# Performance work log

Measured on AMD Instinct MI355X. Metric: run time of the kernel, lower is better.

Reference implementation:

```python
import jax, jax.numpy as jnp
import numpy as np

C, FF, NH = 128, 2048, 8
B, D, H, W = 1, 16, 16, 16
EPS = 1e-5

def setup_inputs() -> dict:
    key = jax.random.key(0)
    ks = jax.random.split(key, 20)
    s = 0.02
    inp = {
        'x': jax.random.normal(ks[0], (B, C, D, H, W), jnp.float32),
        'Wq': jax.random.normal(ks[1], (C, C), jnp.float32) * s,
        'bq': jnp.zeros((C,), jnp.float32),
        'Wk': jax.random.normal(ks[2], (C, C), jnp.float32) * s,
        'bk': jnp.zeros((C,), jnp.float32),
        'Wv': jax.random.normal(ks[3], (C, C), jnp.float32) * s,
        'bv': jnp.zeros((C,), jnp.float32),
        'Wo': jax.random.normal(ks[4], (C, C), jnp.float32) * s,
        'bo': jnp.zeros((C,), jnp.float32),
        'W1': jax.random.normal(ks[5], (FF, C), jnp.float32) * s,
        'b1': jnp.zeros((FF,), jnp.float32),
        'W2': jax.random.normal(ks[6], (C, FF), jnp.float32) * s,
        'b2': jnp.zeros((C,), jnp.float32),
        'g1': jnp.ones((C,), jnp.float32),
        'be1': jnp.zeros((C,), jnp.float32),
        'g2': jnp.ones((C,), jnp.float32),
        'be2': jnp.zeros((C,), jnp.float32),
    }
    return inp

def _layernorm(t, g, b):
    # normalize over last (channel) dim, biased variance like torch LayerNorm
    m = jnp.mean(t, axis=-1, keepdims=True)
    v = jnp.mean(jnp.square(t - m), axis=-1, keepdims=True)
    return (t - m) * jax.lax.rsqrt(v + EPS) * g + b

def reference(x, Wq, bq, Wk, bk, Wv, bv, Wo, bo, W1, b1, W2, b2, g1, be1, g2, be2):
    b_, c, d, h, w = x.shape
    n = d * h * w
    hd = c // NH
    xf = x.reshape(b_, c, n)  # [B,C,N]
    # 1x1 conv3d == per-voxel linear over channels
    q = jnp.einsum('oc,bcn->bon', Wq, xf) + bq[:, None]
    k = jnp.einsum('oc,bcn->bon', Wk, xf) + bk[:, None]
    v = jnp.einsum('oc,bcn->bon', Wv, xf) + bv[:, None]
    q = q.reshape(b_, NH, hd, n)
    k = k.reshape(b_, NH, hd, n)
    v = v.reshape(b_, NH, hd, n)
    scores = jnp.einsum('bhcd,bhce->bhde', q, k) / (hd ** 0.5)  # [B,NH,N,N]
    probs = jax.nn.softmax(scores, axis=-1)
    attn = jnp.einsum('bhde,bhce->bhcd', probs, v).reshape(b_, c, n)
    attn = jnp.einsum('oc,bcn->bon', Wo, attn) + bo[:, None]
    x1 = xf + attn  # residual (dropout = identity at eval)
    x1 = _layernorm(x1.transpose(0, 2, 1), g1, be1)  # [B,N,C]
    hmid = jax.nn.relu(jnp.einsum('fc,bnc->bnf', W1, x1) + b1)
    ffn = jnp.einsum('cf,bnf->bnc', W2, hmid) + b2
    x2 = _layernorm(x1 + ffn, g2, be2)
    return x2.transpose(0, 2, 1).reshape(b_, c, d, h, w)
```

## Files before the change

kernel.cpp:

```cpp
#include <hip/hip_runtime.h>
#include <hip/hip_bf16.h>

typedef __hip_bfloat16 bf16;
typedef short short8 __attribute__((ext_vector_type(8)));
typedef float f32x4 __attribute__((ext_vector_type(4)));

#define C_   128
#define N_   4096
#define NH_  8
#define HD_  16
#define FF_  2048
#define SCALE_Q 0.360673760222241f

__device__ __forceinline__ unsigned short f2bf_bits(float f) {
    bf16 h = __float2bfloat16(f);
    return *reinterpret_cast<unsigned short*>(&h);
}
__device__ __forceinline__ unsigned int pack_trunc(float lo, float hi) {
    return (__float_as_uint(hi) & 0xffff0000u) | (__float_as_uint(lo) >> 16);
}
__device__ __forceinline__ short f2bf_trunc(float f) {
    return (short)(__float_as_uint(f) >> 16);
}
__device__ __forceinline__ float bfs2f(short s) {
    return __uint_as_float(((unsigned int)(unsigned short)s) << 16);
}
__device__ __forceinline__ float fast_exp2(float x) {
    return __builtin_amdgcn_exp2f(x);
}
__device__ __forceinline__ f32x4 mfma16(short8 a, short8 b, f32x4 c) {
    return __builtin_amdgcn_mfma_f32_16x16x32_bf16(a, b, c, 0, 0, 0);
}

__global__ void __launch_bounds__(256) k_prep(
    const float* __restrict__ Wq, const float* __restrict__ Wk,
    const float* __restrict__ Wv, const float* __restrict__ Wo,
    const float* __restrict__ W1, const float* __restrict__ W2,
    const float* __restrict__ x,
    bf16* __restrict__ Wqkvf, bf16* __restrict__ Wof,
    bf16* __restrict__ W1f, bf16* __restrict__ W2f,
    bf16* __restrict__ xTf)
{
    __shared__ float xs[4][512];
    const int tid = threadIdx.x, wave = tid >> 6, lane = tid & 63;
    const int gw = blockIdx.x * 4 + wave;
    const int q = lane >> 4;

    if (gw < 1152) {
        const float* src; bf16* dst; int K, otile, kch, blk;
        if (gw < 96)        { src = 0;  dst = Wqkvf; K = 128;  otile = gw >> 2;          kch = gw & 3;  blk = gw; }
        else if (gw < 128)  { int i = gw - 96;  src = Wo; dst = Wof;  K = 128;  otile = i >> 2; kch = i & 3;  blk = i; }
        else if (gw < 640)  { int i = gw - 128; src = W1; dst = W1f;  K = 128;  otile = i >> 2; kch = i & 3;  blk = i; }
        else                { int i = gw - 640; src = W2; dst = W2f;  K = 2048; otile = i >> 6; kch = i & 63; blk = i; }
        const int o = otile * 16 + (lane & 15);
        const int k0 = kch * 32 + 4 * q;
        const float* row;
        if (gw < 96) {
            row = (o < 128) ? (Wq + o * 128) : (o < 256) ? (Wk + (o - 128) * 128)
                                             : (Wv + (o - 256) * 128);
        } else {
            row = src + (size_t)o * K;
        }
        const float4 A = *(const float4*)(row + k0);
        const float4 B = *(const float4*)(row + k0 + 16);
        short8 v;
        v[0] = f2bf_bits(A.x); v[1] = f2bf_bits(B.x);
        v[2] = f2bf_bits(A.y); v[3] = f2bf_bits(B.y);
        v[4] = f2bf_bits(A.z); v[5] = f2bf_bits(B.z);
        v[6] = f2bf_bits(A.w); v[7] = f2bf_bits(B.w);
        *(short8*)((short*)dst + (size_t)blk * 512 + lane * 8) = v;
    } else {
        const int i = gw - 1152;
        const int n0 = (i >> 2) << 4, c0 = (i & 3) << 5;
        float* S = xs[wave];
        const int cl = lane & 31, ns = (lane >> 5) << 3;
        const float* p = x + (size_t)(c0 + cl) * N_ + n0 + ns;
        *(float4*)(S + cl * 16 + ns)     = *(const float4*)(p);
        *(float4*)(S + cl * 16 + ns + 4) = *(const float4*)(p + 4);
        short8 v;
        #pragma unroll
        for (int j = 0; j < 8; ++j) {
            const int ko = ((j & 1) << 4) + 4 * q + (j >> 1);
            v[j] = f2bf_bits(S[ko * 16 + (lane & 15)]);
        }
        *(short8*)((short*)xTf + (size_t)i * 512 + lane * 8) = v;
    }
}

__global__ void __launch_bounds__(256) k_qkv(
    const bf16* __restrict__ xTf, const bf16* __restrict__ Wqkvf,
    const float* __restrict__ bq, const float* __restrict__ bk, const float* __restrict__ bv,
    bf16* __restrict__ qf, bf16* __restrict__ kf, bf16* __restrict__ vf)
{
    __shared__ short tb[4][512];
    const int tid = threadIdx.x, wave = tid >> 6, lane = tid & 63;
    const int col = lane & 15, quad = lane >> 4;
    const int gw = blockIdx.x * 4 + wave;
    const int rt = gw / 24, ct = gw % 24;
    f32x4 acc = {};
    #pragma unroll
    for (int c = 0; c < 4; ++c) {
        short8 a = *(const short8*)(xTf + ((size_t)(rt * 4 + c) << 9) + lane * 8);
        short8 b = *(const short8*)(Wqkvf + ((size_t)(ct * 4 + c) << 9) + lane * 8);
        acc = mfma16(a, b, acc);
    }
    short* T = tb[wave];
    if (ct < 8) {
        const float bb = bq[ct * 16 + col];
        #pragma unroll
        for (int r = 0; r < 4; ++r)
            T[(col >> 3) * 128 + (quad * 4 + r) * 8 + (col & 7)] =
                f2bf_trunc((acc[r] + bb) * SCALE_Q);
    } else if (ct < 16) {
        const float bb = bk[(ct - 8) * 16 + col];
        #pragma unroll
        for (int r = 0; r < 4; ++r)
            T[(col >> 3) * 128 + (quad * 4 + r) * 8 + (col & 7)] =
                f2bf_trunc(acc[r] + bb);
    } else {
        const float bb = bv[(ct - 16) * 16 + col];
        #pragma unroll
        for (int r = 0; r < 4; ++r) {
            const int ko = quad * 4 + r;
            T[(ko >> 3) * 128 + col * 8 + (ko & 7)] = f2bf_trunc(acc[r] + bb);
        }
    }
    if (lane < 32) {
        short8 w = *(const short8*)(T + lane * 8);
        short* dst;
        if (ct < 8)       dst = (short*)qf + ((ct << 8) + rt) * 256;
        else if (ct < 16) dst = (short*)kf + (((ct - 8) << 8) + rt) * 256;
        else              dst = (short*)vf + ((((ct - 16) << 7) + (rt >> 1)) << 9) + (rt & 1) * 256;
        *(short8*)(dst + lane * 8) = w;
    }
}

__global__ void __launch_bounds__(256)
attn_kernel(const bf16* __restrict__ qf, const bf16* __restrict__ kf,
            const bf16* __restrict__ vf, bf16* __restrict__ af)
{
    __shared__ __align__(16) union {
        unsigned int P[4][2][320];
        float comb[4][64][8];
    } sh;
    const int tid = threadIdx.x, wave = tid >> 6, lane = tid & 63;
    const int col = lane & 15, quad = lane >> 4;
    const int gw = blockIdx.x;
    const int h  = gw >> 8;
    const int tile = gw & 255;
    const f32x4 zero = {};

    short8 aq = {};
    if (quad < 2)
        aq = *(const short8*)(qf + ((size_t)((h << 8) + tile) << 8) + lane * 8);

    f32x4 accO0 = {}, accO1 = {};
    float L[4] = {0.f, 0.f, 0.f, 0.f};

    const int kbeg = wave << 10;
    short* P0 = (short*)&sh.P[wave][0][0];
    short* P1 = (short*)&sh.P[wave][1][0];

    for (int i = 0; i < 32; i += 2) {
        const int mA = kbeg + (i << 5);
        const int mB = mA + 32;

        short8 bkA0 = {}, bkA1 = {}, bkB0 = {}, bkB1 = {};
        if (quad < 2) {
            const bf16* ka = kf + ((size_t)((h << 8) + (mA >> 4)) << 8) + lane * 8;
            bkA0 = *(const short8*)(ka);
            bkA1 = *(const short8*)(ka + 256);
            bkB0 = *(const short8*)(ka + 512);
            bkB1 = *(const short8*)(ka + 768);
        }
        f32x4 s0 = mfma16(aq, bkA0, zero);
        f32x4 s1 = mfma16(aq, bkA1, zero);
        f32x4 s2 = mfma16(aq, bkB0, zero);
        f32x4 s3 = mfma16(aq, bkB1, zero);
        #pragma unroll
        for (int r = 0; r < 4; ++r) {
            const float p0 = fast_exp2(s0[r]);
            const float p1 = fast_exp2(s1[r]);
            const float p2 = fast_exp2(s2[r]);
            const float p3 = fast_exp2(s3[r]);
            L[r] += (p0 + p1) + (p2 + p3);
            const int row = (quad * 4 + r) * 40;
            P0[row + col]      = f2bf_trunc(p0);
            P0[row + 16 + col] = f2bf_trunc(p1);
            P1[row + col]      = f2bf_trunc(p2);
            P1[row + 16 + col] = f2bf_trunc(p3);
        }
        short8 vA = *(const short8*)(vf + ((size_t)((h << 7) + (mA >> 5)) << 9) + lane * 8);
        short8 vB = *(const short8*)(vf + ((size_t)((h << 7) + (mB >> 5)) << 9) + lane * 8);
        short8 ap0 = *(const short8*)(P0 + col * 40 + quad * 8);
        accO0 = mfma16(ap0, vA, accO0);
        short8 ap1 = *(const short8*)(P1 + col * 40 + quad * 8);
        accO1 = mfma16(ap1, vB, accO1);
    }

    f32x4 accO;
    #pragma unroll
    for (int r = 0; r < 4; ++r) accO[r] = accO0[r] + accO1[r];

    __syncthreads();
    #pragma unroll
    for (int r = 0; r < 4; ++r) {
        sh.comb[wave][lane][r]     = accO[r];
        sh.comb[wave][lane][4 + r] = L[r];
    }
    __syncthreads();

    if (wave == 0) {
        #pragma unroll
        for (int r = 0; r < 4; ++r) {
            float O = sh.comb[0][lane][r] + sh.comb[1][lane][r]
                    + sh.comb[2][lane][r] + sh.comb[3][lane][r];
            float l = sh.comb[0][lane][4+r] + sh.comb[1][lane][4+r]
                    + sh.comb[2][lane][4+r] + sh.comb[3][lane][4+r];
            l += __shfl_xor(l, 1); l += __shfl_xor(l, 2);
            l += __shfl_xor(l, 4); l += __shfl_xor(l, 8);
            const int row16 = quad * 4 + r;
            const int pk = (col << 1) + (h & 1);
            af[((tile << 2) + (h >> 1)) * 512 + (((pk >> 3) << 4) + row16) * 8 + (pk & 7)] =
                __float2bfloat16(O / l);
        }
    }
}

__global__ void __launch_bounds__(256, 1)
k_mega(const bf16* __restrict__ af, const bf16* __restrict__ xTf,
       const bf16* __restrict__ Wof, const bf16* __restrict__ W1f, const bf16* __restrict__ W2f,
       const float* __restrict__ bo, const float* __restrict__ b1, const float* __restrict__ b2,
       const float* __restrict__ g1, const float* __restrict__ be1,
       const float* __restrict__ g2, const float* __restrict__ be2,
       float* __restrict__ out)
{
    __shared__ __align__(16) unsigned int Pb[4][2][320];
    __shared__ float comb[96][64];
    const int tid = threadIdx.x, wave = tid >> 6, lane = tid & 63;
    const int col = lane & 15, quad = lane >> 4;
    const int rt = blockIdx.x, n0 = rt << 4;
    const f32x4 zero = {};

    short8 ao[4], xt[4];
    #pragma unroll
    for (int c = 0; c < 4; ++c) {
        ao[c] = *(const short8*)(af  + ((size_t)(rt * 4 + c) << 9) + lane * 8);
        xt[c] = *(const short8*)(xTf + ((size_t)(rt * 4 + c) << 9) + lane * 8);
    }
    f32x4 d[8];
    #pragma unroll
    for (int t = 0; t < 8; ++t) d[t] = zero;
    short8 wa[4], wb[4];
    #pragma unroll
    for (int c = 0; c < 4; ++c)
        wa[c] = *(const short8*)(Wof + ((size_t)(c) << 9) + lane * 8);
    #pragma unroll
    for (int t = 0; t < 8; t += 2) {
        #pragma unroll
        for (int c = 0; c < 4; ++c)
            wb[c] = *(const short8*)(Wof + ((size_t)((t + 1) * 4 + c) << 9) + lane * 8);
        #pragma unroll
        for (int c = 0; c < 4; ++c) d[t] = mfma16(ao[c], wa[c], d[t]);
        if (t + 2 < 8) {
            #pragma unroll
            for (int c = 0; c < 4; ++c)
                wa[c] = *(const short8*)(Wof + ((size_t)((t + 2) * 4 + c) << 9) + lane * 8);
        }
        #pragma unroll
        for (int c = 0; c < 4; ++c) d[t + 1] = mfma16(ao[c], wb[c], d[t + 1]);
    }
    #pragma unroll
    for (int t = 0; t < 8; ++t) {
        const float bt = bo[t * 16 + col];
        #pragma unroll
        for (int r = 0; r < 4; ++r) d[t][r] += bt;
    }

    float x1f[4][8];
    #pragma unroll
    for (int c = 0; c < 4; ++c) {
        unsigned int* Pw = &Pb[wave][c & 1][0];
        const short* Ps = (const short*)Pw;
        #pragma unroll
        for (int r = 0; r < 4; ++r)
            Pw[(quad * 4 + r) * 20 + col] = pack_trunc(d[2 * c][r], d[2 * c + 1][r]);
        short8 ar = *(const short8*)(Ps + col * 40 + quad * 8);
        #pragma unroll
        for (int j = 0; j < 8; ++j)
            x1f[c][j] = bfs2f(ar[j]) + bfs2f(xt[c][j]);
    }

    float s = 0.f, ss = 0.f;
    #pragma unroll
    for (int c = 0; c < 4; ++c)
        #pragma unroll
        for (int j = 0; j < 8; ++j) { s += x1f[c][j]; ss += x1f[c][j] * x1f[c][j]; }
    s  += __shfl_xor(s, 16);  s  += __shfl_xor(s, 32);
    ss += __shfl_xor(ss, 16); ss += __shfl_xor(ss, 32);
    const float m1 = s * (1.f / 128.f);
    const float rstd1 = rsqrtf(ss * (1.f / 128.f) - m1 * m1 + 1e-5f);
    short8 aq1[4];
    #pragma unroll
    for (int c = 0; c < 4; ++c)
        #pragma unroll
        for (int j = 0; j < 8; ++j) {
            const int pos = quad * 8 + j;
            const int ko = ((pos & 1) << 4) + (pos >> 1);
            const int ch = c * 32 + ko;
            aq1[c][j] = f2bf_trunc((x1f[c][j] - m1) * rstd1 * g1[ch] + be1[ch]);
        }

    f32x4 ACC[8];
    #pragma unroll
    for (int t = 0; t < 8; ++t) ACC[t] = zero;
    const int fbase = wave << 4;
    short8 w1a[8], w2a[8], w1b[8], w2b[8];
    #pragma unroll
    for (int c = 0; c < 8; ++c) {
        w1a[c] = *(const short8*)(W1f + ((size_t)(fbase * 8 + c) << 9) + lane * 8);
        w2a[c] = *(const short8*)(W2f + ((size_t)(c * 64 + fbase) << 9) + lane * 8);
    }
    for (int i = 0; i < 16; i += 2) {
        const int f0 = fbase + i, f1 = f0 + 1;
        #pragma unroll
        for (int c = 0; c < 8; ++c) {
            w1b[c] = *(const short8*)(W1f + ((size_t)(f1 * 8 + c) << 9) + lane * 8);
            w2b[c] = *(const short8*)(W2f + ((size_t)(c * 64 + f1) << 9) + lane * 8);
        }
        {
            f32x4 p0 = zero, p1 = zero;
            #pragma unroll
            for (int c = 0; c < 4; ++c) p0 = mfma16(aq1[c], w1a[c], p0);
            #pragma unroll
            for (int c = 0; c < 4; ++c) p1 = mfma16(aq1[c], w1a[4 + c], p1);
            const float bb0 = b1[f0 * 32 + col], bb1 = b1[f0 * 32 + 16 + col];
            unsigned int* Pw = &Pb[wave][0][0];
            #pragma unroll
            for (int r = 0; r < 4; ++r)
                Pw[(quad * 4 + r) * 20 + col] =
                    pack_trunc(fmaxf(p0[r] + bb0, 0.f), fmaxf(p1[r] + bb1, 0.f));
            short8 ah = *(const short8*)((const short*)Pw + col * 40 + quad * 8);
            #pragma unroll
            for (int t = 0; t < 8; ++t) ACC[t] = mfma16(ah, w2a[t], ACC[t]);
        }
        if (i + 2 < 16) {
            const int f2 = f0 + 2;
            #pragma unroll
            for (int c = 0; c < 8; ++c) {
                w1a[c] = *(const short8*)(W1f + ((size_t)(f2 * 8 + c) << 9) + lane * 8);
                w2a[c] = *(const short8*)(W2f + ((size_t)(c * 64 + f2) << 9) + lane * 8);
            }
        }
        {
            f32x4 p0 = zero, p1 = zero;
            #pragma unroll
            for (int c = 0; c < 4; ++c) p0 = mfma16(aq1[c], w1b[c], p0);
            #pragma unroll
            for (int c = 0; c < 4; ++c) p1 = mfma16(aq1[c], w1b[4 + c], p1);
            const float bb0 = b1[f1 * 32 + col], bb1 = b1[f1 * 32 + 16 + col];
            unsigned int* Pw = &Pb[wave][1][0];
            #pragma unroll
            for (int r = 0; r < 4; ++r)
                Pw[(quad * 4 + r) * 20 + col] =
                    pack_trunc(fmaxf(p0[r] + bb0, 0.f), fmaxf(p1[r] + bb1, 0.f));
            short8 ah = *(const short8*)((const short*)Pw + col * 40 + quad * 8);
            #pragma unroll
            for (int t = 0; t < 8; ++t) ACC[t] = mfma16(ah, w2b[t], ACC[t]);
        }
    }

    if (wave) {
        #pragma unroll
        for (int t = 0; t < 8; ++t)
            #pragma unroll
            for (int r = 0; r < 4; ++r)
                comb[(wave - 1) * 32 + t * 4 + r][lane] = ACC[t][r];
    }
    __syncthreads();
    if (wave == 0) {
        #pragma unroll
        for (int t = 0; t < 8; ++t)
            #pragma unroll
            for (int r = 0; r < 4; ++r)
                ACC[t][r] += comb[t * 4 + r][lane] + comb[32 + t * 4 + r][lane]
                           + comb[64 + t * 4 + r][lane];
        short* xb = (short*)&Pb[0][0][0];
        #pragma unroll
        for (int c = 0; c < 4; ++c)
            *(short8*)(xb + (col * 4 + c) * 32 + quad * 8) = aq1[c];
        float t2[8][4];
        #pragma unroll
        for (int t = 0; t < 8; ++t) {
            const int ch = t * 16 + col;
            const int pk = (col << 1) + (t & 1);
            const int c = t >> 1;
            const float bb = b2[ch];
            #pragma unroll
            for (int r = 0; r < 4; ++r)
                t2[t][r] = ACC[t][r] + bb + bfs2f(xb[((quad * 4 + r) * 4 + c) * 32 + pk]);
        }
        #pragma unroll
        for (int r = 0; r < 4; ++r) {
            float S = 0.f, SS = 0.f;
            #pragma unroll
            for (int t = 0; t < 8; ++t) { S += t2[t][r]; SS += t2[t][r] * t2[t][r]; }
            S  += __shfl_xor(S, 1);  S  += __shfl_xor(S, 2);
            S  += __shfl_xor(S, 4);  S  += __shfl_xor(S, 8);
            SS += __shfl_xor(SS, 1); SS += __shfl_xor(SS, 2);
            SS += __shfl_xor(SS, 4); SS += __shfl_xor(SS, 8);
            const float m2 = S * (1.f / 128.f);
            const float rstd2 = rsqrtf(SS * (1.f / 128.f) - m2 * m2 + 1e-5f);
            #pragma unroll
            for (int t = 0; t < 8; ++t) {
                const int ch = t * 16 + col;
                out[(size_t)ch * N_ + n0 + quad * 4 + r] =
                    (t2[t][r] - m2) * rstd2 * g2[ch] + be2[ch];
            }
        }
    }
}

extern "C" void kernel_launch(void* const* d_in, const int* in_sizes, int n_in,
                              void* d_out, int out_size, void* d_ws, size_t ws_size,
                              hipStream_t stream) {
    const float* x   = (const float*)d_in[0];
    const float* Wq  = (const float*)d_in[1];
    const float* bq  = (const float*)d_in[2];
    const float* Wk  = (const float*)d_in[3];
    const float* bk  = (const float*)d_in[4];
    const float* Wv  = (const float*)d_in[5];
    const float* bv  = (const float*)d_in[6];
    const float* Wo  = (const float*)d_in[7];
    const float* bo  = (const float*)d_in[8];
    const float* W1  = (const float*)d_in[9];
    const float* b1  = (const float*)d_in[10];
    const float* W2  = (const float*)d_in[11];
    const float* b2  = (const float*)d_in[12];
    const float* g1  = (const float*)d_in[13];
    const float* be1 = (const float*)d_in[14];
    const float* g2  = (const float*)d_in[15];
    const float* be2 = (const float*)d_in[16];
    float* out = (float*)d_out;

    char* ws = (char*)d_ws;
    bf16* xTf   = (bf16*)(ws + 0);
    bf16* qf    = (bf16*)(ws + 1048576);
    bf16* kf    = (bf16*)(ws + 2097152);
    bf16* vf    = (bf16*)(ws + 3145728);
    bf16* af    = (bf16*)(ws + 4194304);
    bf16* Wqkvf = (bf16*)(ws + 5242880);
    bf16* Wof   = (bf16*)(ws + 5341184);
    bf16* W1f   = (bf16*)(ws + 5373952);
    bf16* W2f   = (bf16*)(ws + 5898240);

    k_prep<<<544, 256, 0, stream>>>(Wq, Wk, Wv, Wo, W1, W2, x, Wqkvf, Wof, W1f, W2f, xTf);
    k_qkv<<<1536, 256, 0, stream>>>(xTf, Wqkvf, bq, bk, bv, qf, kf, vf);
    attn_kernel<<<2048, 256, 0, stream>>>(qf, kf, vf, af);
    k_mega<<<256, 256, 0, stream>>>(af, xTf, Wof, W1f, W2f, bo, b1, b2,
                                    g1, be1, g2, be2, out);
}
```

Before: 144.2 us.

## Spread final FFN reduction/LayerNorm across all waves; pack P stores; direct V writes

In the fused FFN kernel, all four waves now write partial accumulators to shared memory and each wave redundantly computes the row LayerNorm statistics but stores only its own two channel tiles, instead of wave 0 doing all the output work alone. The attention kernel packs pairs of bf16 probabilities into 32-bit LDS stores, halving store count. The QKV kernel writes V directly to global memory in the permuted layout instead of staging through LDS. The trade-off is redundant reduction work per wave, a larger comb buffer, and scattered 2-byte global stores for V.

```diff
diff --git a/kernel.cpp b/kernel.cpp
--- a/kernel.cpp
+++ b/kernel.cpp
@@ -104,34 +104,29 @@
         short8 b = *(const short8*)(Wqkvf + ((size_t)(ct * 4 + c) << 9) + lane * 8);
         acc = mfma16(a, b, acc);
     }
-    short* T = tb[wave];
-    if (ct < 8) {
-        const float bb = bq[ct * 16 + col];
+    if (ct < 16) {
+        short* T = tb[wave];
+        const float bb = (ct < 8) ? bq[ct * 16 + col] : bk[(ct - 8) * 16 + col];
+        const float sc = (ct < 8) ? SCALE_Q : 1.0f;
         #pragma unroll
         for (int r = 0; r < 4; ++r)
             T[(col >> 3) * 128 + (quad * 4 + r) * 8 + (col & 7)] =
-                f2bf_trunc((acc[r] + bb) * SCALE_Q);
-    } else if (ct < 16) {
-        const float bb = bk[(ct - 8) * 16 + col];
-        #pragma unroll
-        for (int r = 0; r < 4; ++r)
-            T[(col >> 3) * 128 + (quad * 4 + r) * 8 + (col & 7)] =
-                f2bf_trunc(acc[r] + bb);
+                f2bf_trunc((acc[r] + bb) * sc);
+        if (lane < 32) {
+            short8 w = *(const short8*)(T + lane * 8);
+            short* dst = (ct < 8) ? (short*)qf + ((ct << 8) + rt) * 256
+                                  : (short*)kf + (((ct - 8) << 8) + rt) * 256;
+            *(short8*)(dst + lane * 8) = w;
+        }
     } else {
         const float bb = bv[(ct - 16) * 16 + col];
+        short* vs = (short*)vf + ((((ct - 16) << 7) + (rt >> 1)) << 9);
         #pragma unroll
         for (int r = 0; r < 4; ++r) {
-            const int ko = quad * 4 + r;
-            T[(ko >> 3) * 128 + col * 8 + (ko & 7)] = f2bf_trunc(acc[r] + bb);
-        }
-    }
-    if (lane < 32) {
-        short8 w = *(const short8*)(T + lane * 8);
-        short* dst;
-        if (ct < 8)       dst = (short*)qf + ((ct << 8) + rt) * 256;
-        else if (ct < 16) dst = (short*)kf + (((ct - 8) << 8) + rt) * 256;
-        else              dst = (short*)vf + ((((ct - 16) << 7) + (rt >> 1)) << 9) + (rt & 1) * 256;
-        *(short8*)(dst + lane * 8) = w;
+            const int local = quad * 4 + r;
+            const int pos = local * 2 + (rt & 1);
+            vs[((pos >> 3) * 16 + col) * 8 + (pos & 7)] = f2bf_trunc(acc[r] + bb);
+        }
     }
 }
 
@@ -158,8 +153,8 @@
     float L[4] = {0.f, 0.f, 0.f, 0.f};
 
     const int kbeg = wave << 10;
-    short* P0 = (short*)&sh.P[wave][0][0];
-    short* P1 = (short*)&sh.P[wave][1][0];
+    unsigned int* P0 = &sh.P[wave][0][0];
+    unsigned int* P1 = &sh.P[wave][1][0];
 
     for (int i = 0; i < 32; i += 2) {
         const int mA = kbeg + (i << 5);
@@ -184,17 +179,14 @@
             const float p2 = fast_exp2(s2[r]);
             const float p3 = fast_exp2(s3[r]);
             L[r] += (p0 + p1) + (p2 + p3);
-            const int row = (quad * 4 + r) * 40;
-            P0[row + col]      = f2bf_trunc(p0);
-            P0[row + 16 + col] = f2bf_trunc(p1);
-            P1[row + col]      = f2bf_trunc(p2);
-            P1[row + 16 + col] = f2bf_trunc(p3);
+            P0[(quad * 4 + r) * 20 + col] = pack_trunc(p0, p1);
+            P1[(quad * 4 + r) * 20 + col] = pack_trunc(p2, p3);
         }
         short8 vA = *(const short8*)(vf + ((size_t)((h << 7) + (mA >> 5)) << 9) + lane * 8);
         short8 vB = *(const short8*)(vf + ((size_t)((h << 7) + (mB >> 5)) << 9) + lane * 8);
-        short8 ap0 = *(const short8*)(P0 + col * 40 + quad * 8);
+        short8 ap0 = *(const short8*)((const short*)P0 + col * 40 + quad * 8);
         accO0 = mfma16(ap0, vA, accO0);
-        short8 ap1 = *(const short8*)(P1 + col * 40 + quad * 8);
+        short8 ap1 = *(const short8*)((const short*)P1 + col * 40 + quad * 8);
         accO1 = mfma16(ap1, vB, accO1);
     }
 
@@ -236,7 +228,7 @@
        float* __restrict__ out)
 {
     __shared__ __align__(16) unsigned int Pb[4][2][320];
-    __shared__ float comb[96][64];
+    __shared__ float comb[128][64];
     const int tid = threadIdx.x, wave = tid >> 6, lane = tid & 63;
     const int col = lane & 15, quad = lane >> 4;
     const int rt = blockIdx.x, n0 = rt << 4;
@@ -370,25 +362,21 @@
         }
     }
 
-    if (wave) {
-        #pragma unroll
-        for (int t = 0; t < 8; ++t)
-            #pragma unroll
-            for (int r = 0; r < 4; ++r)
-                comb[(wave - 1) * 32 + t * 4 + r][lane] = ACC[t][r];
-    }
-    __syncthreads();
+    #pragma unroll
+    for (int t = 0; t < 8; ++t)
+        #pragma unroll
+        for (int r = 0; r < 4; ++r)
+            comb[wave * 32 + t * 4 + r][lane] = ACC[t][r];
     if (wave == 0) {
-        #pragma unroll
-        for (int t = 0; t < 8; ++t)
-            #pragma unroll
-            for (int r = 0; r < 4; ++r)
-                ACC[t][r] += comb[t * 4 + r][lane] + comb[32 + t * 4 + r][lane]
-                           + comb[64 + t * 4 + r][lane];
         short* xb = (short*)&Pb[0][0][0];
         #pragma unroll
         for (int c = 0; c < 4; ++c)
             *(short8*)(xb + (col * 4 + c) * 32 + quad * 8) = aq1[c];
+    }
+    __syncthreads();
+
+    {
+        const short* xb = (const short*)&Pb[0][0][0];
         float t2[8][4];
         #pragma unroll
         for (int t = 0; t < 8; ++t) {
@@ -398,7 +386,9 @@
             const float bb = b2[ch];
             #pragma unroll
             for (int r = 0; r < 4; ++r)
-                t2[t][r] = ACC[t][r] + bb + bfs2f(xb[((quad * 4 + r) * 4 + c) * 32 + pk]);
+                t2[t][r] = comb[t * 4 + r][lane] + comb[32 + t * 4 + r][lane]
+                         + comb[64 + t * 4 + r][lane] + comb[96 + t * 4 + r][lane]
+                         + bb + bfs2f(xb[((quad * 4 + r) * 4 + c) * 32 + pk]);
         }
         #pragma unroll
         for (int r = 0; r < 4; ++r) {
@@ -412,7 +402,8 @@
             const float m2 = S * (1.f / 128.f);
             const float rstd2 = rsqrtf(SS * (1.f / 128.f) - m2 * m2 + 1e-5f);
             #pragma unroll
-            for (int t = 0; t < 8; ++t) {
+            for (int tt = 0; tt < 2; ++tt) {
+                const int t = wave * 2 + tt;
                 const int ch = t * 16 + col;
                 out[(size_t)ch * N_ + n0 + quad * 4 + r] =
                     (t2[t][r] - m2) * rstd2 * g2[ch] + be2[ch];
```

After: 144.8 us. About the same (+0.4%).
